# Kernel optimization log

Hardware: AMD Instinct MI355X
Metric: run time of the kernel (lower is better)

Reference implementation:

```python
import jax, jax.numpy as jnp
import numpy as np

T = 3072          # num tokens
HID = 5120        # hidden_size
H = 16            # num_local_heads
DN = 128          # qk_nope_head_dim
DR = 64           # qk_rope_head_dim
DQK = DN + DR     # qk_head_dim = 192
DV = 128          # v_head_dim
Q_RANK = 1536     # q_lora_rank
KV_RANK = 512     # kv_lora_rank


def rmsnorm(x, w, eps=1e-6):
    var = jnp.mean(jnp.square(x), axis=-1, keepdims=True)
    return x * jax.lax.rsqrt(var + eps) * w


def apply_rope(x, cos, sin):
    # neox-style rotate-half; x [..., DR], cos/sin broadcastable [..., DR//2]
    x1, x2 = jnp.split(x, 2, axis=-1)
    return jnp.concatenate([x1 * cos - x2 * sin, x2 * cos + x1 * sin], axis=-1)


def setup_inputs() -> dict:
    key = jax.random.key(0)
    ks = jax.random.split(key, 8)
    s = 0.02
    positions = jnp.arange(T, dtype=jnp.int32)
    hidden_states = jax.random.normal(ks[0], (T, HID), dtype=jnp.float32)
    llama_4_scaling = jnp.ones((T, 1, 1), dtype=jnp.float32)
    w_q_a = jax.random.normal(ks[1], (HID, Q_RANK), dtype=jnp.float32) * s
    q_a_ln_w = jnp.ones((Q_RANK,), dtype=jnp.float32)
    w_q_b = jax.random.normal(ks[2], (Q_RANK, H * DQK), dtype=jnp.float32) * s
    w_kv_a = jax.random.normal(ks[3], (HID, KV_RANK + DR), dtype=jnp.float32) * s
    kv_a_ln_w = jnp.ones((KV_RANK,), dtype=jnp.float32)
    w_kv_b = jax.random.normal(ks[4], (KV_RANK, H * (DN + DV)), dtype=jnp.float32) * s
    w_o = jax.random.normal(ks[5], (H * DV, HID), dtype=jnp.float32) * s
    # cos/sin cache: [max_pos, DR]; first half cos, second half sin
    inv_freq = 1.0 / (10000.0 ** (jnp.arange(0, DR, 2, dtype=jnp.float32) / DR))
    t = jnp.arange(T, dtype=jnp.float32)
    freqs = t[:, None] * inv_freq[None, :]              # [T, DR//2]
    cos_sin_cache = jnp.concatenate([jnp.cos(freqs), jnp.sin(freqs)], axis=-1)
    return {
        "positions": positions, "hidden_states": hidden_states,
        "llama_4_scaling": llama_4_scaling,
        "w_q_a": w_q_a, "q_a_ln_w": q_a_ln_w, "w_q_b": w_q_b,
        "w_kv_a": w_kv_a, "kv_a_ln_w": kv_a_ln_w, "w_kv_b": w_kv_b,
        "w_o": w_o, "cos_sin_cache": cos_sin_cache,
    }


def reference(positions, hidden_states, llama_4_scaling, w_q_a, q_a_ln_w,
              w_q_b, w_kv_a, kv_a_ln_w, w_kv_b, w_o, cos_sin_cache):
    # ---- Q path: low-rank down/up projection with RMSNorm ----
    q = rmsnorm(hidden_states @ w_q_a, q_a_ln_w) @ w_q_b       # [T, H*DQK]
    q = q.reshape(T, H, DQK)
    q_nope, q_pe = q[..., :DN], q[..., DN:]                    # [T,H,DN],[T,H,DR]

    # ---- KV path: compressed latent + shared rope key ----
    latent = hidden_states @ w_kv_a                            # [T, KV_RANK+DR]
    kv_a = rmsnorm(latent[:, :KV_RANK], kv_a_ln_w)             # [T, KV_RANK]
    k_pe = latent[:, KV_RANK:]                                 # [T, DR] (shared across heads)
    kv = (kv_a @ w_kv_b).reshape(T, H, DN + DV)
    k_nope, v = kv[..., :DN], kv[..., DN:]                     # [T,H,DN],[T,H,DV]

    # ---- partial RoPE on the rope slices only ----
    cs = cos_sin_cache[positions]                              # [T, DR]
    cos, sin = cs[:, :DR // 2], cs[:, DR // 2:]
    q_pe = apply_rope(q_pe, cos[:, None, :], sin[:, None, :])
    k_pe = apply_rope(k_pe, cos, sin)

    q = jnp.concatenate([q_nope, q_pe], axis=-1)               # [T, H, DQK]
    k = jnp.concatenate(
        [k_nope, jnp.broadcast_to(k_pe[:, None, :], (T, H, DR))], axis=-1)

    q = q * llama_4_scaling

    # ---- causal attention (v is zero-padded to DQK in the original;
    #      the pad contributes zeros and is sliced off, so we skip it) ----
    scale = 1.0 / jnp.sqrt(jnp.float32(DQK))
    scores = jnp.einsum('qhd,khd->hqk', q, k) * scale          # [H, T, T]
    causal = positions[:, None] >= positions[None, :]
    scores = jnp.where(causal[None, :, :], scores, jnp.finfo(scores.dtype).min)
    probs = jax.nn.softmax(scores, axis=-1)
    attn = jnp.einsum('hqk,khd->qhd', probs, v)                # [T, H, DV]

    return attn.reshape(T, H * DV) @ w_o                       # [T, HID]
```

## Files before the change

kernel.cpp:

```cpp
#include <hip/hip_runtime.h>
#include <hip/hip_bf16.h>
#include <math.h>

#define T_TOK 3072
#define HID_D 5120
#define NH 16
#define DN 128
#define DR 64
#define DQK 192
#define DV 128
#define QRANK 1536
#define KVRANK 512
#define MERGED_N 2176

typedef __attribute__((ext_vector_type(8))) short short8;
typedef __attribute__((ext_vector_type(4))) float f32x4;
typedef unsigned short u16;

__device__ __forceinline__ u16 f2bf(float f) {
    unsigned int u = __float_as_uint(f);
    unsigned int lsb = (u >> 16) & 1;
    u += 0x7fffu + lsb;
    return (u16)(u >> 16);
}
__device__ __forceinline__ float bf2f(u16 v) {
    return __uint_as_float(((unsigned int)v) << 16);
}

__device__ __forceinline__ void gload_lds16(const u16* g, u16* l) {
    __builtin_amdgcn_global_load_lds((const __attribute__((address_space(1))) void*)g,
                                     (__attribute__((address_space(3))) void*)l, 16, 0, 0);
}

__global__ __launch_bounds__(256) void convert_bf_k(const float* __restrict__ x,
                                                    u16* __restrict__ y, int n4)
{
    const int i = blockIdx.x * 256 + threadIdx.x;
    if (i < n4) {
        float4 v = ((const float4*)x)[i];
        ushort4 o;
        o.x = f2bf(v.x); o.y = f2bf(v.y); o.z = f2bf(v.z); o.w = f2bf(v.w);
        ((ushort4*)y)[i] = o;
    }
}

__global__ __launch_bounds__(256) void transpose_conv_k(const float* __restrict__ W,
                                                        u16* __restrict__ WT,
                                                        int K, int N)
{
    __shared__ float tile[32][33];
    const int n0 = blockIdx.x * 32, k0 = blockIdx.y * 32;
    const int tx = threadIdx.x & 31, ty = threadIdx.x >> 5;
#pragma unroll
    for (int i = 0; i < 32; i += 8) {
        const int nn = n0 + tx;
        tile[ty + i][tx] = (nn < N) ? W[(size_t)(k0 + ty + i) * N + nn] : 0.f;
    }
    __syncthreads();
#pragma unroll
    for (int i = 0; i < 32; i += 8) {
        WT[(size_t)(n0 + ty + i) * K + k0 + tx] = f2bf(tile[tx][ty + i]);
    }
}

template <bool BF16_OUT>
__global__ __launch_bounds__(256) void bgemm_bt_k(
    const u16* __restrict__ A, const u16* __restrict__ BT, void* __restrict__ C,
    int Nreal, int K, int lda, int ldb, int ldc)
{
    __shared__ __attribute__((aligned(16))) u16 As[128 * 32];
    __shared__ __attribute__((aligned(16))) u16 Bs[128 * 32];

    const int tid  = threadIdx.x;
    const int wave = tid >> 6, lane = tid & 63;
    const int quad = lane >> 4, l16 = lane & 15;
    const int wr = (wave >> 1) * 64, wc = (wave & 1) * 64;

    const int gx  = (int)gridDim.x;
    const int nwg = gx * (int)gridDim.y;
    const int lin = (int)blockIdx.y * gx + (int)blockIdx.x;
    const int wid = (lin & 7) * (nwg >> 3) + (lin >> 3);
    const int row0 = (wid / gx) * 128, col0 = (wid % gx) * 128;

    f32x4 acc[4][4];
#pragma unroll
    for (int i = 0; i < 4; ++i)
#pragma unroll
        for (int j = 0; j < 4; ++j) acc[i][j] = (f32x4){0.f, 0.f, 0.f, 0.f};

    const int sr  = tid >> 2;
    const int skc = (tid & 3) * 8;
    const u16* ap0 = A  + (size_t)(row0 + sr)      * lda + skc;
    const u16* ap1 = A  + (size_t)(row0 + sr + 64) * lda + skc;
    const u16* bp0 = BT + (size_t)(col0 + sr)      * ldb + skc;
    const u16* bp1 = BT + (size_t)(col0 + sr + 64) * ldb + skc;
    u16* al0 = As + tid * 8;
    u16* al1 = As + tid * 8 + 64 * 32;
    u16* bl0 = Bs + tid * 8;
    u16* bl1 = Bs + tid * 8 + 64 * 32;

    for (int kt = 0; kt < K; kt += 32) {
        gload_lds16(ap0 + kt, al0);
        gload_lds16(ap1 + kt, al1);
        gload_lds16(bp0 + kt, bl0);
        gload_lds16(bp1 + kt, bl1);
        __syncthreads();

        short8 af[4], bf[4];
#pragma unroll
        for (int mi = 0; mi < 4; ++mi)
            af[mi] = *(const short8*)(As + (wr + mi * 16 + l16) * 32 + quad * 8);
#pragma unroll
        for (int ni = 0; ni < 4; ++ni)
            bf[ni] = *(const short8*)(Bs + (wc + ni * 16 + l16) * 32 + quad * 8);
#pragma unroll
        for (int mi = 0; mi < 4; ++mi)
#pragma unroll
            for (int ni = 0; ni < 4; ++ni)
                acc[mi][ni] = __builtin_amdgcn_mfma_f32_16x16x32_bf16(
                    af[mi], bf[ni], acc[mi][ni], 0, 0, 0);
        __syncthreads();
    }

#pragma unroll
    for (int mi = 0; mi < 4; ++mi) {
#pragma unroll
        for (int ni = 0; ni < 4; ++ni) {
            const int col_g = col0 + wc + ni * 16 + l16;
            if (col_g < Nreal) {
#pragma unroll
                for (int r = 0; r < 4; ++r) {
                    const int row_g = row0 + wr + mi * 16 + quad * 4 + r;
                    if (BF16_OUT)
                        ((u16*)C)[(size_t)row_g * ldc + col_g] = f2bf(acc[mi][ni][r]);
                    else
                        ((float*)C)[(size_t)row_g * ldc + col_g] = acc[mi][ni][r];
                }
            }
        }
    }
}

__global__ __launch_bounds__(256) void rmsnorm_bf_k(const u16* __restrict__ x,
                                                    const float* __restrict__ w,
                                                    u16* __restrict__ y,
                                                    int width, int stride, int off)
{
    const int row = blockIdx.x;
    const u16* xr = x + (size_t)row * stride + off;
    const int nch = width >> 3;
    float ss = 0.f;
    for (int i = threadIdx.x; i < nch; i += 256) {
        short8 v = *(const short8*)(xr + i * 8);
#pragma unroll
        for (int j = 0; j < 8; ++j) { const float f = bf2f((u16)v[j]); ss += f * f; }
    }
    __shared__ float red[256];
    red[threadIdx.x] = ss;
    __syncthreads();
    for (int s2 = 128; s2 > 0; s2 >>= 1) {
        if (threadIdx.x < s2) red[threadIdx.x] += red[threadIdx.x + s2];
        __syncthreads();
    }
    const float scale = rsqrtf(red[0] / (float)width + 1e-6f);
    u16* yr = y + (size_t)row * width;
    for (int i = threadIdx.x; i < nch; i += 256) {
        short8 v = *(const short8*)(xr + i * 8);
        const float4 w0 = *(const float4*)(w + i * 8);
        const float4 w1 = *(const float4*)(w + i * 8 + 4);
        short8 o;
        o[0] = (short)f2bf(bf2f((u16)v[0]) * scale * w0.x);
        o[1] = (short)f2bf(bf2f((u16)v[1]) * scale * w0.y);
        o[2] = (short)f2bf(bf2f((u16)v[2]) * scale * w0.z);
        o[3] = (short)f2bf(bf2f((u16)v[3]) * scale * w0.w);
        o[4] = (short)f2bf(bf2f((u16)v[4]) * scale * w1.x);
        o[5] = (short)f2bf(bf2f((u16)v[5]) * scale * w1.y);
        o[6] = (short)f2bf(bf2f((u16)v[6]) * scale * w1.z);
        o[7] = (short)f2bf(bf2f((u16)v[7]) * scale * w1.w);
        *(short8*)(yr + i * 8) = o;
    }
}

__global__ __launch_bounds__(256) void rope_scale_q_bf_k(const u16* __restrict__ q, const int* __restrict__ positions,
                                  const float* __restrict__ scaling,
                                  const float* __restrict__ cs_cache, u16* __restrict__ qb)
{
    const int t = blockIdx.x;
    const int pos = positions[t];
    const float* cs = cs_cache + (size_t)pos * DR;
    const float s = scaling[t];
    __shared__ float c_sh[32], s_sh[32];
    if (threadIdx.x < 32) {
        c_sh[threadIdx.x] = cs[threadIdx.x];
        s_sh[threadIdx.x] = cs[32 + threadIdx.x];
    }
    __syncthreads();
    const u16* qt = q + (size_t)t * NH * DQK;
    u16* qo = qb + (size_t)t * NH * DQK;
    for (int cc = threadIdx.x; cc < NH * 20; cc += 256) {
        const int hh = cc / 20, c = cc % 20;
        const u16* qr = qt + hh * DQK;
        u16* qw = qo + hh * DQK;
        if (c < 16) {
            short8 v = *(const short8*)(qr + c * 8);
            short8 o;
#pragma unroll
            for (int j = 0; j < 8; ++j) o[j] = (short)f2bf(bf2f((u16)v[j]) * s);
            *(short8*)(qw + c * 8) = o;
        } else {
            const int d0 = (c - 16) * 8;
            short8 x1 = *(const short8*)(qr + 128 + d0);
            short8 x2 = *(const short8*)(qr + 160 + d0);
            short8 o1, o2;
#pragma unroll
            for (int j = 0; j < 8; ++j) {
                const float a = bf2f((u16)x1[j]), b = bf2f((u16)x2[j]);
                const float cv = c_sh[d0 + j], sv = s_sh[d0 + j];
                o1[j] = (short)f2bf((a * cv - b * sv) * s);
                o2[j] = (short)f2bf((b * cv + a * sv) * s);
            }
            *(short8*)(qw + 128 + d0) = o1;
            *(short8*)(qw + 160 + d0) = o2;
        }
    }
}

__global__ void rope_k_bf_k(const u16* __restrict__ qa_lat, u16* __restrict__ kpe,
                            const int* __restrict__ positions,
                            const float* __restrict__ cs_cache)
{
    const int t = blockIdx.x;
    const int d = threadIdx.x;
    if (d >= 32) return;
    const int pos = positions[t];
    const float* cs = cs_cache + (size_t)pos * DR;
    const float c = cs[d], sn = cs[32 + d];
    const u16* lr = qa_lat + (size_t)t * MERGED_N + QRANK + KVRANK;
    const float x1 = bf2f(lr[d]), x2 = bf2f(lr[32 + d]);
    kpe[(size_t)t * DR + d]      = f2bf(x1 * c - x2 * sn);
    kpe[(size_t)t * DR + 32 + d] = f2bf(x2 * c + x1 * sn);
}

__global__ __launch_bounds__(256) void transpose_v_k(const u16* __restrict__ kvb,
                                                     u16* __restrict__ vt)
{
    __shared__ u16 tile[64][72];
    const int t0 = blockIdx.x * 64, d0 = blockIdx.y * 64, h = blockIdx.z;
    const int tid = threadIdx.x;
    for (int cc = tid; cc < 64 * 8; cc += 256) {
        const int row = cc >> 3, c = (cc & 7) * 8;
        *(short8*)&tile[row][c] =
            *(const short8*)(kvb + ((size_t)(t0 + row) * NH + h) * (DN + DV) + DN + d0 + c);
    }
    __syncthreads();
    for (int cc = tid; cc < 64 * 8; cc += 256) {
        const int drow = cc >> 3, c = (cc & 7) * 8;
        short8 s;
#pragma unroll
        for (int j = 0; j < 8; ++j) s[j] = tile[c + j][drow];
        *(short8*)(vt + ((size_t)h * DV + d0 + drow) * T_TOK + t0 + c) = s;
    }
}

#define ATT_BM 128
#define ATT_BN 64
#define KS_STRIDE 200
#define KS_BUF (64 * KS_STRIDE)
__global__ __launch_bounds__(512) void attn_mfma_k(
    const u16* __restrict__ qb, const u16* __restrict__ kvb,
    const u16* __restrict__ kpeb, const u16* __restrict__ vt,
    u16* __restrict__ attnb)
{
    __shared__ u16 Ks[2 * KS_BUF];
    __shared__ u16 Ps[8][16][72];

    const int tid  = threadIdx.x;
    const int wave = tid >> 6;
    const int lane = tid & 63;
    const int quad = lane >> 4;
    const int l16  = lane & 15;

    const int bid   = (int)blockIdx.x;
    const int chunk = bid & 7;
    const int local = bid >> 3;
    const int h     = chunk * 2 + (local & 1);
    const int qblk  = 23 - (local >> 1);
    const int q0    = qblk * ATT_BM;
    const int wrow0 = q0 + wave * 16;
    const int qrow  = wrow0 + l16;

    short8 qf[6];
    {
        const u16* qp = qb + ((size_t)qrow * NH + h) * DQK + quad * 8;
#pragma unroll
        for (int c = 0; c < 6; ++c)
            qf[c] = *(const short8*)(qp + c * 32);
    }

    const u16* gp0; const u16* gp1; const u16* gp2;
    size_t gs0, gs1, gs2;
    int lo0, lo1, lo2;
    {
        const int cc0 = tid,       r0 = cc0 / 24, c0 = cc0 % 24;
        const int cc1 = tid + 512, r1 = cc1 / 24, c1 = cc1 % 24;
        const int cc2 = tid + 1024, r2 = cc2 / 24, c2 = cc2 % 24;
        gp0 = (c0 < 16) ? kvb + ((size_t)r0 * NH + h) * (DN + DV) + c0 * 8
                        : kpeb + (size_t)r0 * DR + (c0 - 16) * 8;
        gs0 = (c0 < 16) ? (size_t)ATT_BN * NH * (DN + DV) : (size_t)ATT_BN * DR;
        lo0 = r0 * KS_STRIDE + c0 * 8;
        gp1 = (c1 < 16) ? kvb + ((size_t)r1 * NH + h) * (DN + DV) + c1 * 8
                        : kpeb + (size_t)r1 * DR + (c1 - 16) * 8;
        gs1 = (c1 < 16) ? (size_t)ATT_BN * NH * (DN + DV) : (size_t)ATT_BN * DR;
        lo1 = r1 * KS_STRIDE + c1 * 8;
        gp2 = (c2 < 16) ? kvb + ((size_t)r2 * NH + h) * (DN + DV) + c2 * 8
                        : kpeb + (size_t)r2 * DR + (c2 - 16) * 8;
        gs2 = (c2 < 16) ? (size_t)ATT_BN * NH * (DN + DV) : (size_t)ATT_BN * DR;
        lo2 = r2 * KS_STRIDE + c2 * 8;
    }

    f32x4 oacc[8];
#pragma unroll
    for (int t = 0; t < 8; ++t) oacc[t] = (f32x4){0.f, 0.f, 0.f, 0.f};
    float m_old[4], l_run[4];
#pragma unroll
    for (int r = 0; r < 4; ++r) { m_old[r] = -1e30f; l_run[r] = 0.f; }

    const u16* vbase = vt + ((size_t)h * DV + l16) * T_TOK + quad * 8;
    const int nkt = 2 * (qblk + 1);

    short8 s0 = *(const short8*)gp0;
    short8 s1 = *(const short8*)gp1;
    short8 s2 = *(const short8*)gp2;
    asm volatile("s_waitcnt vmcnt(0)" ::: "memory");
    *(short8*)(Ks + lo0) = s0;
    *(short8*)(Ks + lo1) = s1;
    *(short8*)(Ks + lo2) = s2;
    s0 = *(const short8*)(gp0 + gs0);
    s1 = *(const short8*)(gp1 + gs1);
    s2 = *(const short8*)(gp2 + gs2);
    asm volatile("s_waitcnt vmcnt(0) lgkmcnt(0)" ::: "memory");
    __builtin_amdgcn_s_barrier();
    __builtin_amdgcn_sched_barrier(0);

    int cur = 0;
    for (int kt = 0; kt < nkt; ++kt) {
        if (kt + 1 < nkt) {
            u16* wp = Ks + (cur ^ 1) * KS_BUF;
            *(short8*)(wp + lo0) = s0;
            *(short8*)(wp + lo1) = s1;
            *(short8*)(wp + lo2) = s2;
        }
        if (kt + 2 < nkt) {
            const size_t o = (size_t)(kt + 2);
            s0 = *(const short8*)(gp0 + o * gs0);
            s1 = *(const short8*)(gp1 + o * gs1);
            s2 = *(const short8*)(gp2 + o * gs2);
        }

        const int k0 = kt * ATT_BN;
        if (k0 <= wrow0 + 15) {
            const u16* kb = Ks + cur * KS_BUF;
            f32x4 sacc[4];
#pragma unroll
            for (int t = 0; t < 4; ++t) sacc[t] = (f32x4){0.f, 0.f, 0.f, 0.f};
            __builtin_amdgcn_s_setprio(1);
#pragma unroll
            for (int t = 0; t < 4; ++t) {
                const u16* kp = kb + (t * 16 + l16) * KS_STRIDE + quad * 8;
#pragma unroll
                for (int c = 0; c < 6; ++c) {
                    short8 bfrag = *(const short8*)(kp + c * 32);
                    sacc[t] = __builtin_amdgcn_mfma_f32_16x16x32_bf16(qf[c], bfrag, sacc[t], 0, 0, 0);
                }
            }
            __builtin_amdgcn_s_setprio(0);
            short8 vv[8];
#pragma unroll
            for (int t = 0; t < 8; ++t)
                vv[t] = *(const short8*)(vbase + (size_t)t * 16 * T_TOK + k0);

            const float sc = 0.07216878364870322f;
            const int rbase = wrow0 + quad * 4;
            if (k0 + ATT_BN - 1 > wrow0) {
#pragma unroll
                for (int t = 0; t < 4; ++t) {
                    const int colg = k0 + t * 16 + l16;
#pragma unroll
                    for (int r = 0; r < 4; ++r) {
                        const float s = sacc[t][r] * sc;
                        sacc[t][r] = (rbase + r >= colg) ? s : -1e30f;
                    }
                }
            } else {
#pragma unroll
                for (int t = 0; t < 4; ++t)
#pragma unroll
                    for (int r = 0; r < 4; ++r) sacc[t][r] *= sc;
            }
            float alpha[4];
#pragma unroll
            for (int r = 0; r < 4; ++r) {
                float mx = fmaxf(fmaxf(sacc[0][r], sacc[1][r]), fmaxf(sacc[2][r], sacc[3][r]));
                mx = fmaxf(mx, __shfl_xor(mx, 1));
                mx = fmaxf(mx, __shfl_xor(mx, 2));
                mx = fmaxf(mx, __shfl_xor(mx, 4));
                mx = fmaxf(mx, __shfl_xor(mx, 8));
                const float mnew = fmaxf(m_old[r], mx);
                alpha[r] = __expf(m_old[r] - mnew);
                float sum = 0.f;
#pragma unroll
                for (int t = 0; t < 4; ++t) {
                    const float p = __expf(sacc[t][r] - mnew);
                    sacc[t][r] = p;
                    sum += p;
                }
                sum += __shfl_xor(sum, 1);
                sum += __shfl_xor(sum, 2);
                sum += __shfl_xor(sum, 4);
                sum += __shfl_xor(sum, 8);
                l_run[r] = l_run[r] * alpha[r] + sum;
                m_old[r] = mnew;
            }
#pragma unroll
            for (int t = 0; t < 4; ++t)
#pragma unroll
                for (int r = 0; r < 4; ++r)
                    Ps[wave][quad * 4 + r][t * 16 + l16] = f2bf(sacc[t][r]);
            short8 ww[8];
#pragma unroll
            for (int t = 0; t < 8; ++t)
                ww[t] = *(const short8*)(vbase + (size_t)t * 16 * T_TOK + k0 + 32);
#pragma unroll
            for (int t = 0; t < 8; ++t)
#pragma unroll
                for (int r = 0; r < 4; ++r)
                    oacc[t][r] *= alpha[r];
            short8 pfrag0 = *(const short8*)&Ps[wave][l16][quad * 8];
            short8 pfrag1 = *(const short8*)&Ps[wave][l16][32 + quad * 8];
            __builtin_amdgcn_s_setprio(1);
#pragma unroll
            for (int t = 0; t < 8; ++t)
                oacc[t] = __builtin_amdgcn_mfma_f32_16x16x32_bf16(pfrag0, vv[t], oacc[t], 0, 0, 0);
#pragma unroll
            for (int t = 0; t < 8; ++t)
                oacc[t] = __builtin_amdgcn_mfma_f32_16x16x32_bf16(pfrag1, ww[t], oacc[t], 0, 0, 0);
            __builtin_amdgcn_s_setprio(0);
        }

        asm volatile("s_waitcnt vmcnt(0) lgkmcnt(0)" ::: "memory");
        __builtin_amdgcn_s_barrier();
        __builtin_amdgcn_sched_barrier(0);
        cur ^= 1;
    }

#pragma unroll
    for (int r = 0; r < 4; ++r) {
        const float linv = 1.f / l_run[r];
        const int row_g = wrow0 + quad * 4 + r;
        u16* op = attnb + (size_t)row_g * (NH * DV) + h * DV;
#pragma unroll
        for (int t = 0; t < 8; ++t)
            op[t * 16 + l16] = f2bf(oacc[t][r] * linv);
    }
}

extern "C" void kernel_launch(void* const* d_in, const int* in_sizes, int n_in,
                              void* d_out, int out_size, void* d_ws, size_t ws_size,
                              hipStream_t stream)
{
    const int*   positions = (const int*)d_in[0];
    const float* hidden    = (const float*)d_in[1];
    const float* scaling   = (const float*)d_in[2];
    const float* w_q_a     = (const float*)d_in[3];
    const float* q_a_ln_w  = (const float*)d_in[4];
    const float* w_q_b     = (const float*)d_in[5];
    const float* w_kv_a    = (const float*)d_in[6];
    const float* kv_a_ln_w = (const float*)d_in[7];
    const float* w_kv_b    = (const float*)d_in[8];
    const float* w_o       = (const float*)d_in[9];
    const float* cs_cache  = (const float*)d_in[10];
    float* out = (float*)d_out;

    char* p = (char*)d_ws;
    auto alloc = [&](size_t bytes) { char* r = p; p += (bytes + 255) & ~(size_t)255; return r; };

    char* regH      = alloc((size_t)T_TOK * HID_D * 2);
    u16*  hidden_bf = (u16*)regH;
    u16*  qraw_bf   = (u16*)regH;
    char* regQ      = alloc((size_t)T_TOK * MERGED_N * 2 + (size_t)T_TOK * QRANK * 2);
    u16*  qa_lat    = (u16*)regQ;
    u16*  q_a_norm  = (u16*)(regQ + (size_t)T_TOK * MERGED_N * 2);
    u16*  qb        = (u16*)regQ;
    u16* kv_a_norm = (u16*)alloc((size_t)T_TOK * KVRANK * 2);
    u16* kpe_bf    = (u16*)alloc((size_t)T_TOK * DR * 2);
    u16* kv_bf     = (u16*)alloc((size_t)T_TOK * NH * (DN + DV) * 2);
    u16* vt        = (u16*)alloc((size_t)NH * DV * T_TOK * 2);
    u16* attnb     = (u16*)alloc((size_t)T_TOK * NH * DV * 2);
    u16* wqakva_bt = (u16*)alloc((size_t)MERGED_N * HID_D * 2);
    u16* wqb_bt    = (u16*)alloc((size_t)(NH * DQK) * QRANK * 2);
    u16* wkvb_bt   = (u16*)alloc((size_t)(NH * (DN + DV)) * KVRANK * 2);
    u16* wo_bt     = (u16*)alloc((size_t)HID_D * (NH * DV) * 2);

    const dim3 blk(256);

    convert_bf_k<<<dim3((T_TOK * HID_D / 4 + 255) / 256), blk, 0, stream>>>(
        hidden, hidden_bf, T_TOK * HID_D / 4);
    transpose_conv_k<<<dim3(QRANK / 32, HID_D / 32), blk, 0, stream>>>(
        w_q_a, wqakva_bt, HID_D, QRANK);
    transpose_conv_k<<<dim3(640 / 32, HID_D / 32), blk, 0, stream>>>(
        w_kv_a, wqakva_bt + (size_t)QRANK * HID_D, HID_D, KVRANK + DR);
    transpose_conv_k<<<dim3(NH * DQK / 32, QRANK / 32), blk, 0, stream>>>(w_q_b, wqb_bt, QRANK, NH * DQK);
    transpose_conv_k<<<dim3(NH * (DN + DV) / 32, KVRANK / 32), blk, 0, stream>>>(w_kv_b, wkvb_bt, KVRANK, NH * (DN + DV));
    transpose_conv_k<<<dim3(HID_D / 32, NH * DV / 32), blk, 0, stream>>>(w_o, wo_bt, NH * DV, HID_D);

    bgemm_bt_k<true><<<dim3(MERGED_N / 128, T_TOK / 128), blk, 0, stream>>>(
        hidden_bf, wqakva_bt, qa_lat, QRANK + KVRANK + DR, HID_D, HID_D, HID_D, MERGED_N);
    rope_k_bf_k<<<dim3(T_TOK), dim3(64), 0, stream>>>(qa_lat, kpe_bf, positions, cs_cache);
    rmsnorm_bf_k<<<dim3(T_TOK), blk, 0, stream>>>(qa_lat, q_a_ln_w, q_a_norm, QRANK, MERGED_N, 0);
    rmsnorm_bf_k<<<dim3(T_TOK), blk, 0, stream>>>(qa_lat, kv_a_ln_w, kv_a_norm, KVRANK, MERGED_N, QRANK);
    bgemm_bt_k<true><<<dim3(NH * DQK / 128, T_TOK / 128), blk, 0, stream>>>(
        q_a_norm, wqb_bt, qraw_bf, NH * DQK, QRANK, QRANK, QRANK, NH * DQK);
    rope_scale_q_bf_k<<<dim3(T_TOK), blk, 0, stream>>>(qraw_bf, positions, scaling, cs_cache, qb);
    bgemm_bt_k<true><<<dim3(NH * (DN + DV) / 128, T_TOK / 128), blk, 0, stream>>>(
        kv_a_norm, wkvb_bt, kv_bf, NH * (DN + DV), KVRANK, KVRANK, KVRANK, NH * (DN + DV));
    transpose_v_k<<<dim3(T_TOK / 64, DV / 64, NH), blk, 0, stream>>>(kv_bf, vt);
    attn_mfma_k<<<dim3(384), dim3(512), 0, stream>>>(qb, kv_bf, kpe_bf, vt, attnb);
    bgemm_bt_k<false><<<dim3(HID_D / 128, T_TOK / 128), blk, 0, stream>>>(
        attnb, wo_bt, out, HID_D, NH * DV, NH * DV, NH * DV, HID_D);
}
```

Measured before the change: 770.2 us.

## Double-buffer LDS tiles in bf16 GEMM to overlap global loads with MFMA

Splits the GEMM main loop into stage and compute helpers and adds a second pair of LDS buffers. The next K-tile's direct-to-LDS loads are issued before computing on the current tile, with one waitcnt plus barrier per iteration instead of two barriers. The aim is to hide global load latency behind MFMA work, at the cost of doubled LDS per block, which may lower occupancy.

```diff
diff --git a/kernel.cpp b/kernel.cpp
--- a/kernel.cpp
+++ b/kernel.cpp
@@ -63,13 +63,44 @@
     }
 }
 
+__device__ __forceinline__ void gemm_stage(const u16* a0, const u16* a1,
+                                           const u16* b0, const u16* b1,
+                                           u16* As, u16* Bs, int tid)
+{
+    gload_lds16(a0, As + tid * 8);
+    gload_lds16(a1, As + tid * 8 + 64 * 32);
+    gload_lds16(b0, Bs + tid * 8);
+    gload_lds16(b1, Bs + tid * 8 + 64 * 32);
+}
+
+__device__ __forceinline__ void gemm_compute(const u16* As, const u16* Bs,
+                                             int wr, int wc, int l16, int quad,
+                                             f32x4 acc[4][4])
+{
+    short8 af[4], bf[4];
+#pragma unroll
+    for (int mi = 0; mi < 4; ++mi)
+        af[mi] = *(const short8*)(As + (wr + mi * 16 + l16) * 32 + quad * 8);
+#pragma unroll
+    for (int ni = 0; ni < 4; ++ni)
+        bf[ni] = *(const short8*)(Bs + (wc + ni * 16 + l16) * 32 + quad * 8);
+#pragma unroll
+    for (int mi = 0; mi < 4; ++mi)
+#pragma unroll
+        for (int ni = 0; ni < 4; ++ni)
+            acc[mi][ni] = __builtin_amdgcn_mfma_f32_16x16x32_bf16(
+                af[mi], bf[ni], acc[mi][ni], 0, 0, 0);
+}
+
 template <bool BF16_OUT>
 __global__ __launch_bounds__(256) void bgemm_bt_k(
     const u16* __restrict__ A, const u16* __restrict__ BT, void* __restrict__ C,
     int Nreal, int K, int lda, int ldb, int ldc)
 {
-    __shared__ __attribute__((aligned(16))) u16 As[128 * 32];
-    __shared__ __attribute__((aligned(16))) u16 Bs[128 * 32];
+    __shared__ __attribute__((aligned(16))) u16 As0[128 * 32];
+    __shared__ __attribute__((aligned(16))) u16 Bs0[128 * 32];
+    __shared__ __attribute__((aligned(16))) u16 As1[128 * 32];
+    __shared__ __attribute__((aligned(16))) u16 Bs1[128 * 32];
 
     const int tid  = threadIdx.x;
     const int wave = tid >> 6, lane = tid & 63;
@@ -94,32 +125,27 @@
     const u16* ap1 = A  + (size_t)(row0 + sr + 64) * lda + skc;
     const u16* bp0 = BT + (size_t)(col0 + sr)      * ldb + skc;
     const u16* bp1 = BT + (size_t)(col0 + sr + 64) * ldb + skc;
-    u16* al0 = As + tid * 8;
-    u16* al1 = As + tid * 8 + 64 * 32;
-    u16* bl0 = Bs + tid * 8;
-    u16* bl1 = Bs + tid * 8 + 64 * 32;
-
-    for (int kt = 0; kt < K; kt += 32) {
-        gload_lds16(ap0 + kt, al0);
-        gload_lds16(ap1 + kt, al1);
-        gload_lds16(bp0 + kt, bl0);
-        gload_lds16(bp1 + kt, bl1);
-        __syncthreads();
-
-        short8 af[4], bf[4];
-#pragma unroll
-        for (int mi = 0; mi < 4; ++mi)
-            af[mi] = *(const short8*)(As + (wr + mi * 16 + l16) * 32 + quad * 8);
-#pragma unroll
-        for (int ni = 0; ni < 4; ++ni)
-            bf[ni] = *(const short8*)(Bs + (wc + ni * 16 + l16) * 32 + quad * 8);
-#pragma unroll
-        for (int mi = 0; mi < 4; ++mi)
-#pragma unroll
-            for (int ni = 0; ni < 4; ++ni)
-                acc[mi][ni] = __builtin_amdgcn_mfma_f32_16x16x32_bf16(
-                    af[mi], bf[ni], acc[mi][ni], 0, 0, 0);
-        __syncthreads();
+
+    const int nk = K >> 5;
+    gemm_stage(ap0, ap1, bp0, bp1, As0, Bs0, tid);
+    asm volatile("s_waitcnt vmcnt(0)" ::: "memory");
+    __builtin_amdgcn_s_barrier();
+    __builtin_amdgcn_sched_barrier(0);
+
+    for (int kt = 0; kt < nk; ++kt) {
+        const int nxt = (kt + 1) << 5;
+        if ((kt & 1) == 0) {
+            if (kt + 1 < nk)
+                gemm_stage(ap0 + nxt, ap1 + nxt, bp0 + nxt, bp1 + nxt, As1, Bs1, tid);
+            gemm_compute(As0, Bs0, wr, wc, l16, quad, acc);
+        } else {
+            if (kt + 1 < nk)
+                gemm_stage(ap0 + nxt, ap1 + nxt, bp0 + nxt, bp1 + nxt, As0, Bs0, tid);
+            gemm_compute(As1, Bs1, wr, wc, l16, quad, acc);
+        }
+        asm volatile("s_waitcnt vmcnt(0)" ::: "memory");
+        __builtin_amdgcn_s_barrier();
+        __builtin_amdgcn_sched_barrier(0);
     }
 
 #pragma unroll
```

Result: slower. 820.6 us (+6.5%).

## Split attention KV range in two per block and merge partials in combine kernel

Applied to the files above, without the earlier changes.

Each query block/head pair is now processed by two workgroups, each covering half of the causal KV tiles. The halves write unnormalized fp32 partial outputs plus running max and sum, and a new combine kernel merges them with log-sum-exp weights into bf16. This doubles the grid to raise occupancy and shorten the longest (late-query) blocks. The cost is fp32 partial-output traffic and an extra kernel launch. The workspace for one partial is aliased onto the hidden-state bf16 region.

```diff
diff --git a/kernel.cpp b/kernel.cpp
--- a/kernel.cpp
+++ b/kernel.cpp
@@ -269,7 +269,8 @@
 __global__ __launch_bounds__(512) void attn_mfma_k(
     const u16* __restrict__ qb, const u16* __restrict__ kvb,
     const u16* __restrict__ kpeb, const u16* __restrict__ vt,
-    u16* __restrict__ attnb)
+    float* __restrict__ o0, float* __restrict__ o1,
+    float* __restrict__ ml0, float* __restrict__ ml1)
 {
     __shared__ u16 Ks[2 * KS_BUF];
     __shared__ u16 Ps[8][16][72];
@@ -283,8 +284,9 @@
     const int bid   = (int)blockIdx.x;
     const int chunk = bid & 7;
     const int local = bid >> 3;
-    const int h     = chunk * 2 + (local & 1);
-    const int qblk  = 23 - (local >> 1);
+    const int qblk  = 23 - (local >> 2);
+    const int h     = chunk * 2 + ((local >> 1) & 1);
+    const int sK    = local & 1;
     const int q0    = qblk * ATT_BM;
     const int wrow0 = q0 + wave * 16;
     const int qrow  = wrow0 + l16;
@@ -326,31 +328,33 @@
     for (int r = 0; r < 4; ++r) { m_old[r] = -1e30f; l_run[r] = 0.f; }
 
     const u16* vbase = vt + ((size_t)h * DV + l16) * T_TOK + quad * 8;
-    const int nkt = 2 * (qblk + 1);
-
-    short8 s0 = *(const short8*)gp0;
-    short8 s1 = *(const short8*)gp1;
-    short8 s2 = *(const short8*)gp2;
+    const int halfn = qblk + 1;
+    const int ktBeg = sK * halfn;
+    const int ktEnd = ktBeg + halfn;
+
+    short8 s0 = *(const short8*)(gp0 + (size_t)ktBeg * gs0);
+    short8 s1 = *(const short8*)(gp1 + (size_t)ktBeg * gs1);
+    short8 s2 = *(const short8*)(gp2 + (size_t)ktBeg * gs2);
     asm volatile("s_waitcnt vmcnt(0)" ::: "memory");
     *(short8*)(Ks + lo0) = s0;
     *(short8*)(Ks + lo1) = s1;
     *(short8*)(Ks + lo2) = s2;
-    s0 = *(const short8*)(gp0 + gs0);
-    s1 = *(const short8*)(gp1 + gs1);
-    s2 = *(const short8*)(gp2 + gs2);
+    s0 = *(const short8*)(gp0 + (size_t)(ktBeg + 1) * gs0);
+    s1 = *(const short8*)(gp1 + (size_t)(ktBeg + 1) * gs1);
+    s2 = *(const short8*)(gp2 + (size_t)(ktBeg + 1) * gs2);
     asm volatile("s_waitcnt vmcnt(0) lgkmcnt(0)" ::: "memory");
     __builtin_amdgcn_s_barrier();
     __builtin_amdgcn_sched_barrier(0);
 
     int cur = 0;
-    for (int kt = 0; kt < nkt; ++kt) {
-        if (kt + 1 < nkt) {
+    for (int kt = ktBeg; kt < ktEnd; ++kt) {
+        if (kt + 1 < ktEnd) {
             u16* wp = Ks + (cur ^ 1) * KS_BUF;
             *(short8*)(wp + lo0) = s0;
             *(short8*)(wp + lo1) = s1;
             *(short8*)(wp + lo2) = s2;
         }
-        if (kt + 2 < nkt) {
+        if (kt + 2 < ktEnd) {
             const size_t o = (size_t)(kt + 2);
             s0 = *(const short8*)(gp0 + o * gs0);
             s1 = *(const short8*)(gp1 + o * gs1);
@@ -453,15 +457,43 @@
         cur ^= 1;
     }
 
+    float* opart = sK ? o1 : o0;
+    float* mlp   = sK ? ml1 : ml0;
 #pragma unroll
     for (int r = 0; r < 4; ++r) {
-        const float linv = 1.f / l_run[r];
         const int row_g = wrow0 + quad * 4 + r;
-        u16* op = attnb + (size_t)row_g * (NH * DV) + h * DV;
+        float* op = opart + ((size_t)row_g * NH + h) * DV;
 #pragma unroll
         for (int t = 0; t < 8; ++t)
-            op[t * 16 + l16] = f2bf(oacc[t][r] * linv);
-    }
+            op[t * 16 + l16] = oacc[t][r];
+        if (l16 == 0) {
+            float* mp = mlp + ((size_t)row_g * NH + h) * 2;
+            mp[0] = m_old[r];
+            mp[1] = l_run[r];
+        }
+    }
+}
+
+__global__ __launch_bounds__(256) void attn_combine_k(
+    const float* __restrict__ o0, const float* __restrict__ o1,
+    const float* __restrict__ ml0, const float* __restrict__ ml1,
+    u16* __restrict__ attnb)
+{
+    const int row = blockIdx.x * 8 + (threadIdx.x >> 5);
+    const int c   = (threadIdx.x & 31) * 4;
+    const float2 a = *(const float2*)(ml0 + (size_t)row * 2);
+    const float2 b = *(const float2*)(ml1 + (size_t)row * 2);
+    const float m  = fmaxf(a.x, b.x);
+    const float wA = __expf(a.x - m), wB = __expf(b.x - m);
+    const float linv = 1.f / (a.y * wA + b.y * wB);
+    const float4 va = *(const float4*)(o0 + (size_t)row * DV + c);
+    const float4 vb = *(const float4*)(o1 + (size_t)row * DV + c);
+    ushort4 o;
+    o.x = f2bf((va.x * wA + vb.x * wB) * linv);
+    o.y = f2bf((va.y * wA + vb.y * wB) * linv);
+    o.z = f2bf((va.z * wA + vb.z * wB) * linv);
+    o.w = f2bf((va.w * wA + vb.w * wB) * linv);
+    *(ushort4*)(attnb + (size_t)row * DV + c) = o;
 }
 
 extern "C" void kernel_launch(void* const* d_in, const int* in_sizes, int n_in,
@@ -487,6 +519,7 @@
     char* regH      = alloc((size_t)T_TOK * HID_D * 2);
     u16*  hidden_bf = (u16*)regH;
     u16*  qraw_bf   = (u16*)regH;
+    float* attn_o0  = (float*)regH;
     char* regQ      = alloc((size_t)T_TOK * MERGED_N * 2 + (size_t)T_TOK * QRANK * 2);
     u16*  qa_lat    = (u16*)regQ;
     u16*  q_a_norm  = (u16*)(regQ + (size_t)T_TOK * MERGED_N * 2);
@@ -500,6 +533,9 @@
     u16* wqb_bt    = (u16*)alloc((size_t)(NH * DQK) * QRANK * 2);
     u16* wkvb_bt   = (u16*)alloc((size_t)(NH * (DN + DV)) * KVRANK * 2);
     u16* wo_bt     = (u16*)alloc((size_t)HID_D * (NH * DV) * 2);
+    float* attn_o1 = (float*)alloc((size_t)T_TOK * NH * DV * 4);
+    float* attn_ml0 = (float*)alloc((size_t)T_TOK * NH * 2 * 4);
+    float* attn_ml1 = (float*)alloc((size_t)T_TOK * NH * 2 * 4);
 
     const dim3 blk(256);
 
@@ -524,7 +560,10 @@
     bgemm_bt_k<true><<<dim3(NH * (DN + DV) / 128, T_TOK / 128), blk, 0, stream>>>(
         kv_a_norm, wkvb_bt, kv_bf, NH * (DN + DV), KVRANK, KVRANK, KVRANK, NH * (DN + DV));
     transpose_v_k<<<dim3(T_TOK / 64, DV / 64, NH), blk, 0, stream>>>(kv_bf, vt);
-    attn_mfma_k<<<dim3(384), dim3(512), 0, stream>>>(qb, kv_bf, kpe_bf, vt, attnb);
+    attn_mfma_k<<<dim3(768), dim3(512), 0, stream>>>(qb, kv_bf, kpe_bf, vt,
+                                                     attn_o0, attn_o1, attn_ml0, attn_ml1);
+    attn_combine_k<<<dim3(T_TOK * NH / 8), blk, 0, stream>>>(
+        attn_o0, attn_o1, attn_ml0, attn_ml1, attnb);
     bgemm_bt_k<false><<<dim3(HID_D / 128, T_TOK / 128), blk, 0, stream>>>(
         attnb, wo_bt, out, HID_D, NH * DV, NH * DV, NH * DV, HID_D);
 }
```

Measured after the change: 759.6 us. No clear change (-1.4%).
